# Kernel optimization log

Measured on AMD Instinct MI355X. Metric: run time of the kernel, lower is better.

Reference implementation:

```python
import jax, jax.numpy as jnp
import numpy as np

B, C, H, W = 16, 512, 64, 64
K = 32


def setup_inputs() -> dict:
    key = jax.random.key(0)
    k1, k2, k3 = jax.random.split(key, 3)
    std = 1.0 / (64 * C) ** 0.5
    x = jax.random.normal(k1, (B, C, H, W), dtype=jnp.float32)
    codewords = jax.random.uniform(k2, (K, C), dtype=jnp.float32, minval=-std, maxval=std)
    scale = jax.random.uniform(k3, (K,), dtype=jnp.float32, minval=-1.0, maxval=0.0)
    return {"x": x, "codewords": codewords, "scale": scale}


def reference(x, codewords, scale):
    b, c, h, w = x.shape
    # (b, n, c) with n = h*w spatial positions
    xf = x.reshape(b, c, h * w).transpose(0, 2, 1)
    x2 = jnp.sum(xf * xf, axis=-1)                       # (b, n)
    c2 = jnp.sum(codewords * codewords, axis=-1)          # (k,)
    xc = jnp.einsum('bnc,kc->bnk', xf, codewords)         # (b, n, k)
    logits = scale[None, None, :] * (x2[:, :, None] - 2.0 * xc + c2[None, None, :])
    A = jax.nn.softmax(logits, axis=2)                    # (b, n, k)
    # sum_n A[b,n,k] * (x[b,n,c] - codewords[k,c])
    encoded = jnp.einsum('bnk,bnc->bkc', A, xf) - jnp.einsum('bnk,kc->bkc', A, codewords)
    return encoded
```

## Files before the change

kernel.cpp:

```cpp
#include <hip/hip_runtime.h>
#include <hip/hip_bf16.h>
#include <math.h>

#define BB 16
#define CC 512
#define NN 4096
#define KK 32

typedef __attribute__((ext_vector_type(8))) short short8;
typedef __attribute__((ext_vector_type(4))) float float4v;

static __device__ __forceinline__ unsigned short f2bf(float f) {
  unsigned u = __float_as_uint(f);
  u += 0x7FFF + ((u >> 16) & 1);
  return (unsigned short)(u >> 16);
}


__global__ __launch_bounds__(256) void prep_kernel(
    const float* __restrict__ cw, unsigned short* __restrict__ cwB,
    float* __restrict__ c2, float* __restrict__ asum, float* __restrict__ out) {
  int gid = blockIdx.x * 256 + threadIdx.x;
  float4v z = {0.f, 0.f, 0.f, 0.f};
  float4v* o4 = (float4v*)out;
#pragma unroll
  for (int j = 0; j < 4; ++j) o4[gid + j * 16384] = z;
  if (gid < BB * KK) asum[gid] = 0.f;
  cwB[gid] = f2bf(cw[gid]);
  __shared__ float c2p[KK][8];
  if (blockIdx.x == 0) {
    int k = threadIdx.x >> 3, j = threadIdx.x & 7;
    const float* row = cw + k * CC + j * 64;
    float s = 0.f;
    for (int i = 0; i < 64; ++i) s = fmaf(row[i], row[i], s);
    c2p[k][j] = s;
    __syncthreads();
    if (threadIdx.x < KK) {
      float t = 0.f;
      for (int j2 = 0; j2 < 8; ++j2) t += c2p[threadIdx.x][j2];
      c2[threadIdx.x] = t;
    }
  }
}

#define XP 72
__global__ __launch_bounds__(256, 2) void fused_kernel(
    const float* __restrict__ x, const unsigned short* __restrict__ cwB,
    const float* __restrict__ c2g, const float* __restrict__ scale,
    float* __restrict__ out, float* __restrict__ asum) {
  const int b = blockIdx.x >> 5;
  const int chunk = blockIdx.x & 31;
  const int t = threadIdx.x;
  const int w = t >> 6;
  const int l = t & 63;
  const int l15 = l & 15;
  const int q = l >> 4;

  __shared__ char smem[512 * XP * 2 + 32 * XP * 2 + 256];
  unsigned short* Xl = (unsigned short*)smem;
  unsigned short* As = (unsigned short*)(smem + 512 * XP * 2);
  float* Sx2p = (float*)(smem + 512 * XP * 2);
  float* Sx2 = (float*)(smem + 512 * XP * 2 + 32 * XP * 2);

  const float* xb0 = x + (size_t)b * CC * NN + chunk * 128;

  const float sc0 = scale[l15], sc1 = scale[16 + l15];
  const float cc0 = c2g[l15], cc1 = c2g[16 + l15];

  float4v acc[8][2];
#pragma unroll
  for (int ct = 0; ct < 8; ++ct)
#pragma unroll
    for (int m = 0; m < 2; ++m) acc[ct][m] = (float4v){0.f, 0.f, 0.f, 0.f};
  float s0acc = 0.f, s1acc = 0.f;

  const int f4 = t & 15;
  const int cr = t >> 4;

  for (int sub = 0; sub < 2; ++sub) {
    const float* xb = xb0 + sub * 64;

    {
      float4v x2p = {0.f, 0.f, 0.f, 0.f};
#pragma unroll 8
      for (int i = 0; i < 32; ++i) {
        const int c = cr + 16 * i;
        float4v v = *(const float4v*)(xb + (size_t)c * NN + 4 * f4);
        x2p.x = fmaf(v.x, v.x, x2p.x);
        x2p.y = fmaf(v.y, v.y, x2p.y);
        x2p.z = fmaf(v.z, v.z, x2p.z);
        x2p.w = fmaf(v.w, v.w, x2p.w);
        unsigned p0 = (unsigned)f2bf(v.x) | ((unsigned)f2bf(v.y) << 16);
        unsigned p1 = (unsigned)f2bf(v.z) | ((unsigned)f2bf(v.w) << 16);
        *(uint2*)&Xl[c * XP + 4 * f4] = make_uint2(p0, p1);
      }
      *(float4v*)&Sx2p[cr * 68 + 4 * f4] = x2p;
    }
    __syncthreads();
    if (t < 64) {
      float s = 0.f;
#pragma unroll
      for (int r = 0; r < 16; ++r) s += Sx2p[r * 68 + t];
      Sx2[t] = s;
    }
    __syncthreads();

    float4v p0 = {0.f, 0.f, 0.f, 0.f};
    float4v p1 = {0.f, 0.f, 0.f, 0.f};
    const int nrow = w * 16 + l15;
    for (int cs = 0; cs < 512; cs += 32) {
      const int cb = cs + q * 8;
      short8 af;
#pragma unroll
      for (int j = 0; j < 8; ++j) af[j] = (short)Xl[(cb + j) * XP + nrow];
      short8 b0 = *(const short8*)(cwB + (size_t)l15 * CC + cb);
      short8 b1 = *(const short8*)(cwB + (size_t)(16 + l15) * CC + cb);
      p0 = __builtin_amdgcn_mfma_f32_16x16x32_bf16(af, b0, p0, 0, 0, 0);
      p1 = __builtin_amdgcn_mfma_f32_16x16x32_bf16(af, b1, p1, 0, 0, 0);
    }

    float a0[4], a1[4];
#pragma unroll
    for (int r = 0; r < 4; ++r) {
      const float xx = Sx2[w * 16 + 4 * q + r];
      float l0 = sc0 * (xx - 2.f * p0[r] + cc0);
      float l1 = sc1 * (xx - 2.f * p1[r] + cc1);
      float m = fmaxf(l0, l1);
      m = fmaxf(m, __shfl_xor(m, 1));
      m = fmaxf(m, __shfl_xor(m, 2));
      m = fmaxf(m, __shfl_xor(m, 4));
      m = fmaxf(m, __shfl_xor(m, 8));
      float e0 = __expf(l0 - m), e1 = __expf(l1 - m);
      float s = e0 + e1;
      s += __shfl_xor(s, 1);
      s += __shfl_xor(s, 2);
      s += __shfl_xor(s, 4);
      s += __shfl_xor(s, 8);
      float inv = 1.0f / s;
      a0[r] = e0 * inv;
      a1[r] = e1 * inv;
    }
    s0acc += a0[0] + a0[1] + a0[2] + a0[3];
    s1acc += a1[0] + a1[1] + a1[2] + a1[3];

    {
      unsigned p00 = (unsigned)f2bf(a0[0]) | ((unsigned)f2bf(a0[1]) << 16);
      unsigned p01 = (unsigned)f2bf(a0[2]) | ((unsigned)f2bf(a0[3]) << 16);
      unsigned p10 = (unsigned)f2bf(a1[0]) | ((unsigned)f2bf(a1[1]) << 16);
      unsigned p11 = (unsigned)f2bf(a1[2]) | ((unsigned)f2bf(a1[3]) << 16);
      const int nc = w * 16 + 4 * q;
      *(uint2*)&As[l15 * XP + nc] = make_uint2(p00, p01);
      *(uint2*)&As[(16 + l15) * XP + nc] = make_uint2(p10, p11);
    }
    __syncthreads();

#pragma unroll
    for (int s = 0; s < 2; ++s) {
      const int nb = s * 32 + q * 8;
      short8 am0 = *(const short8*)&As[l15 * XP + nb];
      short8 am1 = *(const short8*)&As[(16 + l15) * XP + nb];
#pragma unroll
      for (int ct = 0; ct < 8; ++ct) {
        const int c = w * 128 + ct * 16 + l15;
        short8 bx = *(const short8*)&Xl[c * XP + nb];
        acc[ct][0] = __builtin_amdgcn_mfma_f32_16x16x32_bf16(am0, bx, acc[ct][0], 0, 0, 0);
        acc[ct][1] = __builtin_amdgcn_mfma_f32_16x16x32_bf16(am1, bx, acc[ct][1], 0, 0, 0);
      }
    }
    __syncthreads();
  }

#pragma unroll
  for (int ct = 0; ct < 8; ++ct) {
    const int c = w * 128 + ct * 16 + l15;
#pragma unroll
    for (int m = 0; m < 2; ++m)
#pragma unroll
      for (int r = 0; r < 4; ++r) {
        int k = 16 * m + 4 * q + r;
        atomicAdd(&out[((size_t)(b * KK + k)) * CC + c], acc[ct][m][r]);
      }
  }
  s0acc += __shfl_xor(s0acc, 16);
  s0acc += __shfl_xor(s0acc, 32);
  s1acc += __shfl_xor(s1acc, 16);
  s1acc += __shfl_xor(s1acc, 32);
  if (q == 0) {
    atomicAdd(&asum[b * KK + l15], s0acc);
    atomicAdd(&asum[b * KK + 16 + l15], s1acc);
  }
}

__global__ __launch_bounds__(256) void finalize_kernel(
    float* __restrict__ out, const float* __restrict__ asum,
    const float* __restrict__ cw) {
  int idx = blockIdx.x * 256 + threadIdx.x;
  int b = idx >> 12;
  int k = (idx >> 7) & 31;
  int c4 = idx & 127;
  float4v o = ((float4v*)out)[idx];
  float4v wv = ((const float4v*)cw)[k * 128 + c4];
  float a = asum[b * KK + k];
  o.x -= a * wv.x;
  o.y -= a * wv.y;
  o.z -= a * wv.z;
  o.w -= a * wv.w;
  ((float4v*)out)[idx] = o;
}

extern "C" void kernel_launch(void* const* d_in, const int* in_sizes, int n_in,
                              void* d_out, int out_size, void* d_ws, size_t ws_size,
                              hipStream_t stream) {
  const float* x = (const float*)d_in[0];
  const float* cw = (const float*)d_in[1];
  const float* scale = (const float*)d_in[2];
  float* out = (float*)d_out;
  char* ws = (char*)d_ws;

  float* c2 = (float*)ws;
  unsigned short* cwB = (unsigned short*)(ws + 128);
  float* asum = (float*)(ws + 32896);

  prep_kernel<<<64, 256, 0, stream>>>(cw, cwB, c2, asum, out);
  fused_kernel<<<512, 256, 0, stream>>>(x, cwB, c2, scale, out, asum);
  finalize_kernel<<<256, 256, 0, stream>>>(out, asum, cw);
}
```

Baseline: 233.0 us.

## Replace output atomics with per-block partials and a reduction kernel

Each fused block now writes its 32x512 partial encoding to a workspace buffer with plain stores instead of atomically adding into the output. The finalize kernel becomes a reduction that sums the 32 partials per batch and then subtracts the codeword term. Separately, the bf16 codewords are stored in a permuted channel order so the first MFMA reads X columns in pairs, which changes the LDS access pattern. This removes atomic contention and the output-zeroing pass, at the cost of an extra 32 MB of partial writes and reads through the workspace.

After: 228.2 us. -2.1%, faster.

```diff
diff --git a/kernel.cpp b/kernel.cpp
--- a/kernel.cpp
+++ b/kernel.cpp
@@ -18,15 +18,19 @@
 
 
 __global__ __launch_bounds__(256) void prep_kernel(
-    const float* __restrict__ cw, unsigned short* __restrict__ cwB,
-    float* __restrict__ c2, float* __restrict__ asum, float* __restrict__ out) {
+    const float* __restrict__ cw, unsigned short* __restrict__ cwP,
+    float* __restrict__ c2, float* __restrict__ asum) {
   int gid = blockIdx.x * 256 + threadIdx.x;
-  float4v z = {0.f, 0.f, 0.f, 0.f};
-  float4v* o4 = (float4v*)out;
-#pragma unroll
-  for (int j = 0; j < 4; ++j) o4[gid + j * 16384] = z;
   if (gid < BB * KK) asum[gid] = 0.f;
-  cwB[gid] = f2bf(cw[gid]);
+  {
+    int k = gid >> 9;
+    int cc = gid & 511;
+    int cs = cc & ~31;
+    int w5 = cc & 31;
+    int q = w5 >> 3, j = w5 & 7;
+    int src_c = cs + 2 * q + (j & 1) + ((j >> 1) << 3);
+    cwP[gid] = f2bf(cw[k * CC + src_c]);
+  }
   __shared__ float c2p[KK][8];
   if (blockIdx.x == 0) {
     int k = threadIdx.x >> 3, j = threadIdx.x & 7;
@@ -45,9 +49,9 @@
 
 #define XP 72
 __global__ __launch_bounds__(256, 2) void fused_kernel(
-    const float* __restrict__ x, const unsigned short* __restrict__ cwB,
+    const float* __restrict__ x, const unsigned short* __restrict__ cwP,
     const float* __restrict__ c2g, const float* __restrict__ scale,
-    float* __restrict__ out, float* __restrict__ asum) {
+    float* __restrict__ partials, float* __restrict__ asum) {
   const int b = blockIdx.x >> 5;
   const int chunk = blockIdx.x & 31;
   const int t = threadIdx.x;
@@ -109,12 +113,15 @@
     float4v p1 = {0.f, 0.f, 0.f, 0.f};
     const int nrow = w * 16 + l15;
     for (int cs = 0; cs < 512; cs += 32) {
-      const int cb = cs + q * 8;
+      const int cb2 = cs + 2 * q;
       short8 af;
 #pragma unroll
-      for (int j = 0; j < 8; ++j) af[j] = (short)Xl[(cb + j) * XP + nrow];
-      short8 b0 = *(const short8*)(cwB + (size_t)l15 * CC + cb);
-      short8 b1 = *(const short8*)(cwB + (size_t)(16 + l15) * CC + cb);
+      for (int j = 0; j < 8; ++j) {
+        const int c = cb2 + (j & 1) + ((j >> 1) << 3);
+        af[j] = (short)Xl[c * XP + nrow];
+      }
+      short8 b0 = *(const short8*)(cwP + (size_t)l15 * CC + cs + q * 8);
+      short8 b1 = *(const short8*)(cwP + (size_t)(16 + l15) * CC + cs + q * 8);
       p0 = __builtin_amdgcn_mfma_f32_16x16x32_bf16(af, b0, p0, 0, 0, 0);
       p1 = __builtin_amdgcn_mfma_f32_16x16x32_bf16(af, b1, p1, 0, 0, 0);
     }
@@ -170,6 +177,7 @@
     __syncthreads();
   }
 
+  float* pout = partials + (size_t)blockIdx.x * KK * CC;
 #pragma unroll
   for (int ct = 0; ct < 8; ++ct) {
     const int c = w * 128 + ct * 16 + l15;
@@ -178,7 +186,7 @@
 #pragma unroll
       for (int r = 0; r < 4; ++r) {
         int k = 16 * m + 4 * q + r;
-        atomicAdd(&out[((size_t)(b * KK + k)) * CC + c], acc[ct][m][r]);
+        pout[k * CC + c] = acc[ct][m][r];
       }
   }
   s0acc += __shfl_xor(s0acc, 16);
@@ -191,14 +199,24 @@
   }
 }
 
-__global__ __launch_bounds__(256) void finalize_kernel(
-    float* __restrict__ out, const float* __restrict__ asum,
-    const float* __restrict__ cw) {
+__global__ __launch_bounds__(256) void reduce_kernel(
+    const float* __restrict__ partials, const float* __restrict__ asum,
+    const float* __restrict__ cw, float* __restrict__ out) {
   int idx = blockIdx.x * 256 + threadIdx.x;
   int b = idx >> 12;
   int k = (idx >> 7) & 31;
   int c4 = idx & 127;
-  float4v o = ((float4v*)out)[idx];
+
+  float4v o = {0.f, 0.f, 0.f, 0.f};
+  const float4v* pb = (const float4v*)partials + ((size_t)(b * 32) * KK + k) * 128 + c4;
+#pragma unroll 8
+  for (int p = 0; p < 32; ++p) {
+    float4v v = pb[(size_t)p * KK * 128];
+    o.x += v.x;
+    o.y += v.y;
+    o.z += v.z;
+    o.w += v.w;
+  }
   float4v wv = ((const float4v*)cw)[k * 128 + c4];
   float a = asum[b * KK + k];
   o.x -= a * wv.x;
@@ -218,10 +236,11 @@
   char* ws = (char*)d_ws;
 
   float* c2 = (float*)ws;
-  unsigned short* cwB = (unsigned short*)(ws + 128);
+  unsigned short* cwP = (unsigned short*)(ws + 128);
   float* asum = (float*)(ws + 32896);
-
-  prep_kernel<<<64, 256, 0, stream>>>(cw, cwB, c2, asum, out);
-  fused_kernel<<<512, 256, 0, stream>>>(x, cwB, c2, scale, out, asum);
-  finalize_kernel<<<256, 256, 0, stream>>>(out, asum, cw);
-}
+  float* partials = (float*)(ws + 35072);
+
+  prep_kernel<<<64, 256, 0, stream>>>(cw, cwP, c2, asum);
+  fused_kernel<<<512, 256, 0, stream>>>(x, cwP, c2, scale, partials, asum);
+  reduce_kernel<<<256, 256, 0, stream>>>(partials, asum, cw, out);
+}
```
